# Kernel optimization log

Measured on AMD Instinct MI355X. Metric: run time of the kernel, lower is better.

## Reference

```python
import jax, jax.numpy as jnp
import numpy as np

IMG_SIZE = 416.0
CLASS_NUM = 80
NUM_ANCH = 3
MAX_GT = 64  # fixed padding for per-image valid GT boxes (original uses a variable-size python loop)


def _bce_logits(x, t):
    # BCEWithLogits, elementwise: softplus(x) - x*t  (numerically stable)
    return jax.nn.softplus(x) - x * t


def _make_noobj_mask(pred_boxes, targets):
    # pred_boxes: [B,G,G,3,4] in pixel units; targets: [B,G,G,3,85]
    B, G = pred_boxes.shape[0], pred_boxes.shape[1]
    N = G * G * NUM_ANCH
    conf = targets[..., 4].reshape(B, N)
    boxes = targets[..., 0:4].reshape(B, N, 4)
    # gather up to MAX_GT ground-truth boxes per image (conf>0 are the valid ones)
    top_conf, idx = jax.lax.top_k(conf, MAX_GT)            # [B,M]
    gt = jnp.take_along_axis(boxes, idx[..., None], axis=1)  # [B,M,4]
    valid = top_conf > 0.0                                   # [B,M]

    p = pred_boxes.reshape(B, N, 4)
    pxy = p[:, :, None, 0:2]   # [B,N,1,2]
    pwh = p[:, :, None, 2:4]
    gxy = gt[:, None, :, 0:2]  # [B,1,M,2]
    gwh = gt[:, None, :, 2:4]

    imin = jnp.maximum(pxy - pwh / 2, gxy - gwh / 2)
    imax = jnp.minimum(pxy + pwh / 2, gxy + gwh / 2)
    iwh = jnp.maximum(imax - imin, 0.0)
    inter = iwh[..., 0] * iwh[..., 1]                        # [B,N,M]
    area_p = pwh[..., 0] * pwh[..., 1]
    area_g = gwh[..., 0] * gwh[..., 1]
    iou = inter / (area_p + area_g - inter + 1e-9)
    iou = jnp.where(valid[:, None, :], iou, 0.0)
    best_iou = jnp.max(iou, axis=-1)                         # [B,N]
    noobj = (best_iou < 0.6).astype(pred_boxes.dtype)
    return noobj.reshape(B, G, G, NUM_ANCH)


def reference(preds, targets, anchors):
    B, G = preds.shape[0], preds.shape[1]
    ratio = IMG_SIZE / G
    p = preds.reshape(B, G, G, NUM_ANCH, 5 + CLASS_NUM)
    box_xy_raw, box_wh_raw, conf_logit, cls_logit = jnp.split(p, [2, 4, 5], axis=-1)

    # grid offsets: offset[i,j] = (j, i)
    gx, gy = jnp.meshgrid(jnp.arange(G, dtype=preds.dtype), jnp.arange(G, dtype=preds.dtype))
    offset = jnp.stack([gx, gy], axis=-1).reshape(G, G, 1, 2)

    sig_xy = jax.nn.sigmoid(box_xy_raw)
    box_xy = (sig_xy + offset) * ratio                 # pixel units
    box_wh = jnp.exp(box_wh_raw) * anchors             # (anchors/ratio)*ratio = anchors
    pred_boxes = jnp.concatenate([box_xy, box_wh], axis=-1)

    preds_xy = box_xy / ratio - offset                 # == sig_xy
    true_xy = targets[..., 0:2] / ratio - offset
    true_wh = targets[..., 2:4] / anchors
    preds_wh = box_wh / anchors
    true_wh = jnp.where(true_wh == 0.0, 1.0, true_wh)
    preds_wh = jnp.where(preds_wh == 0.0, 1.0, preds_wh)
    true_wh = jnp.log(jnp.clip(true_wh, 1e-9, 1e9))
    preds_wh = jnp.log(jnp.clip(preds_wh, 1e-9, 1e9))

    obj = (targets[..., 4] > 0.0).astype(preds.dtype)  # [B,G,G,3]
    obj_e = obj[..., None]
    scale = 2.0 - targets[..., 2:3] / IMG_SIZE * targets[..., 3:4] / IMG_SIZE  # [B,G,G,3,1]

    txty_loss = jnp.sum(obj_e * (preds_xy - true_xy) ** 2 * scale) / B
    twth_loss = jnp.sum(obj_e * (preds_wh - true_wh) ** 2 * scale) / B

    noobj = _make_noobj_mask(pred_boxes, targets)      # [B,G,G,3]
    noobj_conf_mask = (1.0 - obj) * noobj
    conf_t = targets[..., 4:5]
    noobj_conf_loss = jnp.sum(noobj_conf_mask[..., None] * _bce_logits(conf_logit, conf_t)) / B
    obj_conf_loss = jnp.sum(obj_e * _bce_logits(conf_logit, conf_t)) / B
    class_loss = jnp.sum(obj_e * _bce_logits(cls_logit, targets[..., 5:])) / B

    total_loss = txty_loss + twth_loss + noobj_conf_loss + obj_conf_loss + class_loss
    return (txty_loss, twth_loss, noobj_conf_loss, obj_conf_loss, class_loss, total_loss)


def setup_inputs() -> dict:
    key = jax.random.key(0)
    ks = jax.random.split(key, 5)
    B, G, A, C = 32, 52, NUM_ANCH, CLASS_NUM
    N = G * G * A
    M_OBJ = 40  # GT boxes per image (< MAX_GT)
    preds = jax.random.normal(ks[0], (B, G, G, A * (5 + C)), jnp.float32) * 0.5
    idx = jax.random.randint(ks[1], (B, M_OBJ), 0, N)
    xy = jax.random.uniform(ks[2], (B, M_OBJ, 2), jnp.float32, 0.0, IMG_SIZE)
    wh = jax.random.uniform(ks[3], (B, M_OBJ, 2), jnp.float32, 16.0, 128.0)
    cid = jax.random.randint(ks[4], (B, M_OBJ), 0, C)
    onehot = jax.nn.one_hot(cid, C, dtype=jnp.float32)
    vals = jnp.concatenate([xy, wh, jnp.ones((B, M_OBJ, 1), jnp.float32), onehot], axis=-1)
    t = jnp.zeros((B, N, 5 + C), jnp.float32)
    t = t.at[jnp.arange(B)[:, None], idx].set(vals)
    targets = t.reshape(B, G, G, A, 5 + C)
    anchors = jnp.array([[10.0, 13.0], [16.0, 30.0], [33.0, 23.0]], jnp.float32)
    return {"preds": preds, "targets": targets, "anchors": anchors}
```

## Files before the change

### kernel.cpp

```cpp
#include <hip/hip_runtime.h>
#include <math.h>

#define GSZ 52
#define NA 3
#define NCLS 80
#define CH 85
#define NCA (GSZ*GSZ*NA)
#define MAXGT 64
#define MCHUNK 32

__device__ __forceinline__ float softplus_fast(float x) {
    return fmaxf(x, 0.0f) + __logf(1.0f + __expf(-fabsf(x)));
}

__global__ void k_init(int* cnt, int B) {
    if (threadIdx.x < B) cnt[threadIdx.x] = 0;
}

__device__ __forceinline__ void emit_gt(const float* __restrict__ tg, size_t glob,
                                        int* cnt, float4* __restrict__ gtbox,
                                        int2* __restrict__ gtinfo) {
    const float* r = tg + glob * CH;
    int b    = (int)(glob / NCA);
    int nloc = (int)(glob - (size_t)b * NCA);
    int cid = 0;
#pragma unroll 16
    for (int c = 0; c < NCLS; c++) if (r[5 + c] > 0.5f) cid = c;
    int pos = atomicAdd(cnt + b, 1);
    if (pos < MAXGT) {
        gtbox[b * MAXGT + pos]  = make_float4(r[0], r[1], r[2], r[3]);
        gtinfo[b * MAXGT + pos] = make_int2(nloc, cid);
    }
}

__global__ void k_gt(const float* __restrict__ tg, int nrec, int* cnt,
                     float4* __restrict__ gtbox, int2* __restrict__ gtinfo) {
    int tid = threadIdx.x;
    size_t g0 = (size_t)blockIdx.x * 512 + tid;
    size_t g1 = g0 + 256;
    float c0 = (g0 < (size_t)nrec) ? tg[g0 * CH + 4] : 0.0f;
    float c1 = (g1 < (size_t)nrec) ? tg[g1 * CH + 4] : 0.0f;
    if (c0 > 0.0f) emit_gt(tg, g0, cnt, gtbox, gtinfo);
    if (c1 > 0.0f) emit_gt(tg, g1, cnt, gtbox, gtinfo);
}

__global__ void k_noobj(const float* __restrict__ pr,
                        const float* __restrict__ anchors,
                        const int* __restrict__ cnt,
                        const float4* __restrict__ gtbox,
                        const int2* __restrict__ gtinfo,
                        float* __restrict__ partial) {
    __shared__ float4 sbox[MAXGT];
    __shared__ int    sidx[MAXGT];
    __shared__ float  swsum[4];

    int b   = blockIdx.y;
    int tid = threadIdx.x;
    int n   = blockIdx.x * 256 + tid;

    int m = min(cnt[b], MAXGT);
    if (tid < m) {
        sbox[tid] = gtbox[b * MAXGT + tid];
        sidx[tid] = gtinfo[b * MAXGT + tid].x;
    }
    __syncthreads();

    float v = 0.0f;
    if (n < NCA) {
        const float* r = pr + ((size_t)b * NCA + n) * CH;
        float r0 = r[0], r1 = r[1], r2 = r[2], r3 = r[3], pc = r[4];

        int a    = n % NA;
        int cell = n / NA;
        int gi = cell / GSZ, gj = cell % GSZ;
        float aw = anchors[2 * a], ah = anchors[2 * a + 1];
        float sx = __builtin_amdgcn_rcpf(1.0f + __expf(-r0));
        float sy = __builtin_amdgcn_rcpf(1.0f + __expf(-r1));
        float bx = (sx + (float)gj) * 8.0f;
        float by = (sy + (float)gi) * 8.0f;
        float bw = __expf(r2) * aw;
        float bh = __expf(r3) * ah;

        float px0 = bx - bw * 0.5f, px1 = bx + bw * 0.5f;
        float py0 = by - bh * 0.5f, py1 = by + bh * 0.5f;
        float areap = bw * bh;

        float best = 0.0f;
        bool isobj = false;
        for (int k = 0; k < m; k++) {
            float4 g = sbox[k];
            isobj |= (sidx[k] == n);
            float ix = fminf(px1, g.x + g.z * 0.5f) - fmaxf(px0, g.x - g.z * 0.5f);
            float iy = fminf(py1, g.y + g.w * 0.5f) - fmaxf(py0, g.y - g.w * 0.5f);
            float inter = fmaxf(ix, 0.0f) * fmaxf(iy, 0.0f);
            float u = areap + g.z * g.w - inter + 1e-9f;
            best = fmaxf(best, inter * __builtin_amdgcn_rcpf(u));
        }
        if (!isobj && best < 0.6f) v = softplus_fast(pc);
    }

    int lane = tid & 63;
    int wv   = tid >> 6;
    for (int off = 32; off > 0; off >>= 1) v += __shfl_down(v, off);
    if (lane == 0) swsum[wv] = v;
    __syncthreads();
    if (tid == 0) {
        int bid = blockIdx.y * gridDim.x + blockIdx.x;
        partial[bid] = swsum[0] + swsum[1] + swsum[2] + swsum[3];
    }
}

__global__ void k_cls(const float* __restrict__ pr,
                      const float* __restrict__ anchors,
                      const int* __restrict__ cnt,
                      const float4* __restrict__ gtbox,
                      const int2* __restrict__ gtinfo,
                      float4* __restrict__ cls4) {
    int tid  = threadIdx.x;
    int wv   = tid >> 6;
    int lane = tid & 63;
    int slot = blockIdx.x * 4 + wv;
    int b = slot >> 6;
    int k = slot & (MAXGT - 1);

    float4 resv = make_float4(0.f, 0.f, 0.f, 0.f);
    int m = min(cnt[b], MAXGT);
    if (k < m) {
        float4 g  = gtbox[slot];
        int2 info = gtinfo[slot];
        int n = info.x, cid = info.y;
        size_t rec = (size_t)b * NCA + n;
        const float* rp = pr + rec * CH;
        const float* cl = rp + 5;

        float x0 = cl[lane];
        float cls = softplus_fast(x0) - (lane == cid ? x0 : 0.0f);
        if (lane < NCLS - 64) {
            float x1 = cl[64 + lane];
            cls += softplus_fast(x1) - ((64 + lane) == cid ? x1 : 0.0f);
        }
        for (int off = 32; off > 0; off >>= 1) cls += __shfl_down(cls, off);

        if (lane == 0) {
            float r0 = rp[0], r1 = rp[1], r2 = rp[2], r3 = rp[3], pc = rp[4];
            int a    = n % NA;
            int cell = n / NA;
            int gi = cell / GSZ, gj = cell % GSZ;
            float aw = anchors[2 * a], ah = anchors[2 * a + 1];

            float sx = __builtin_amdgcn_rcpf(1.0f + __expf(-r0));
            float sy = __builtin_amdgcn_rcpf(1.0f + __expf(-r1));
            float pbx = (sx + (float)gj) * 8.0f;
            float pby = (sy + (float)gi) * 8.0f;
            float pbz = __expf(r2) * aw;
            float pbw = __expf(r3) * ah;

            float scale = 2.0f - (g.z * (1.0f / 416.0f)) * (g.w * (1.0f / 416.0f));
            float dx = (pbx * 0.125f - (float)gj) - (g.x * 0.125f - (float)gj);
            float dy = (pby * 0.125f - (float)gi) - (g.y * 0.125f - (float)gi);
            float txty = (dx * dx + dy * dy) * scale;

            float rw = __builtin_amdgcn_rcpf(aw), rh = __builtin_amdgcn_rcpf(ah);
            float pwr = fminf(fmaxf(pbz * rw, 1e-9f), 1e9f);
            float phr = fminf(fmaxf(pbw * rh, 1e-9f), 1e9f);
            float twr = fminf(fmaxf(g.z  * rw, 1e-9f), 1e9f);
            float thr = fminf(fmaxf(g.w  * rh, 1e-9f), 1e9f);
            float dw = __logf(pwr) - __logf(twr);
            float dh = __logf(phr) - __logf(thr);
            float twth = (dw * dw + dh * dh) * scale;

            float obj = softplus_fast(pc) - pc;
            resv = make_float4(txty, twth, obj, cls);
        }
    }
    if (lane == 0) cls4[slot] = resv;
}

__global__ void k_final(const float* __restrict__ partial, int np,
                        const float4* __restrict__ cls4, int ns,
                        int B, float* __restrict__ out) {
    __shared__ double sred[4 * 5];
    int tid = threadIdx.x;
    double acc[5] = {0, 0, 0, 0, 0};
    for (int i = tid; i < np; i += 256) acc[2] += (double)partial[i];
    for (int i = tid; i < ns; i += 256) {
        float4 v = cls4[i];
        acc[0] += (double)v.x; acc[1] += (double)v.y;
        acc[3] += (double)v.z; acc[4] += (double)v.w;
    }
    int lane = tid & 63;
    int wv   = tid >> 6;
#pragma unroll
    for (int i = 0; i < 5; i++) {
        double v = acc[i];
        for (int off = 32; off > 0; off >>= 1) v += __shfl_down(v, off);
        if (lane == 0) sred[wv * 5 + i] = v;
    }
    __syncthreads();
    if (tid == 0) {
        double tot = 0.0;
#pragma unroll
        for (int i = 0; i < 5; i++) {
            double r = (sred[i] + sred[5 + i] + sred[10 + i] + sred[15 + i]) / (double)B;
            out[i] = (float)r;
            tot += r;
        }
        out[5] = (float)tot;
    }
}

extern "C" void kernel_launch(void* const* d_in, const int* in_sizes, int n_in,
                              void* d_out, int out_size, void* d_ws, size_t ws_size,
                              hipStream_t stream) {
    const float* preds   = (const float*)d_in[0];
    const float* targets = (const float*)d_in[1];
    const float* anchors = (const float*)d_in[2];
    float* out = (float*)d_out;

    int B = in_sizes[0] / (NCA * CH);
    int nrec = B * NCA;
    int gt_blocks = (nrec + 511) / 512;
    int np = MCHUNK * B;
    int ns = B * MAXGT;

    char* ws = (char*)d_ws;
    size_t off = 0;
    int*    cnt     = (int*)(ws + off);      off += 128;
    float4* gtbox   = (float4*)(ws + off);   off += (size_t)ns * sizeof(float4);
    int2*   gtinfo  = (int2*)(ws + off);     off += (size_t)ns * sizeof(int2);
    float*  partial = (float*)(ws + off);    off += (size_t)np * sizeof(float);
    off = (off + 15) & ~(size_t)15;
    float4* cls4    = (float4*)(ws + off);   off += (size_t)ns * sizeof(float4);

    k_init<<<1, 64, 0, stream>>>(cnt, B);
    k_gt<<<gt_blocks, 256, 0, stream>>>(targets, nrec, cnt, gtbox, gtinfo);
    dim3 grid(MCHUNK, B);
    k_noobj<<<grid, 256, 0, stream>>>(preds, anchors, cnt, gtbox, gtinfo, partial);
    k_cls<<<ns / 4, 256, 0, stream>>>(preds, anchors, cnt, gtbox, gtinfo, cls4);
    k_final<<<1, 256, 0, stream>>>(partial, np, cls4, ns, B, out);
}
```

Before: 197.1 us.

## Decode pred boxes during GT scan and merge noobj and class kernels

The GT-scan kernel now also reads the first five prediction channels of every record and writes the decoded box and confidence logit to a compact workspace. The noobj and class/box-loss kernels are merged into a single launch that reads these compact decoded values instead of the strided 85-float records. The aim is to cut one launch and turn strided prediction reads in the IoU pass into coalesced float4 reads. The cost is extra workspace traffic for the decoded arrays and a scan that now touches both input tensors.

Result: no change. 196.6 us (-0.2%).

```diff
diff --git a/kernel.cpp b/kernel.cpp
--- a/kernel.cpp
+++ b/kernel.cpp
@@ -8,6 +8,7 @@
 #define NCA (GSZ*GSZ*NA)
 #define MAXGT 64
 #define MCHUNK 32
+#define CLSBLK 16
 
 __device__ __forceinline__ float softplus_fast(float x) {
     return fmaxf(x, 0.0f) + __logf(1.0f + __expf(-fabsf(x)));
@@ -17,12 +18,12 @@
     if (threadIdx.x < B) cnt[threadIdx.x] = 0;
 }
 
-__device__ __forceinline__ void emit_gt(const float* __restrict__ tg, size_t glob,
+__device__ __forceinline__ void emit_gt(const float* __restrict__ tg, int glob,
                                         int* cnt, float4* __restrict__ gtbox,
                                         int2* __restrict__ gtinfo) {
-    const float* r = tg + glob * CH;
-    int b    = (int)(glob / NCA);
-    int nloc = (int)(glob - (size_t)b * NCA);
+    const float* r = tg + (size_t)glob * CH;
+    int b    = glob / NCA;
+    int nloc = glob - b * NCA;
     int cid = 0;
 #pragma unroll 16
     for (int c = 0; c < NCLS; c++) if (r[5 + c] > 0.5f) cid = c;
@@ -33,147 +34,144 @@
     }
 }
 
-__global__ void k_gt(const float* __restrict__ tg, int nrec, int* cnt,
-                     float4* __restrict__ gtbox, int2* __restrict__ gtinfo) {
-    int tid = threadIdx.x;
-    size_t g0 = (size_t)blockIdx.x * 512 + tid;
-    size_t g1 = g0 + 256;
-    float c0 = (g0 < (size_t)nrec) ? tg[g0 * CH + 4] : 0.0f;
-    float c1 = (g1 < (size_t)nrec) ? tg[g1 * CH + 4] : 0.0f;
-    if (c0 > 0.0f) emit_gt(tg, g0, cnt, gtbox, gtinfo);
-    if (c1 > 0.0f) emit_gt(tg, g1, cnt, gtbox, gtinfo);
-}
-
-__global__ void k_noobj(const float* __restrict__ pr,
-                        const float* __restrict__ anchors,
-                        const int* __restrict__ cnt,
-                        const float4* __restrict__ gtbox,
-                        const int2* __restrict__ gtinfo,
-                        float* __restrict__ partial) {
-    __shared__ float4 sbox[MAXGT];
-    __shared__ int    sidx[MAXGT];
-    __shared__ float  swsum[4];
-
+__global__ void k_scan(const float* __restrict__ tg, const float* __restrict__ pr,
+                       const float* __restrict__ anchors, int nrec, int* cnt,
+                       float4* __restrict__ gtbox, int2* __restrict__ gtinfo,
+                       float4* __restrict__ boxdec, float* __restrict__ confdec) {
+    int rec = blockIdx.x * 256 + threadIdx.x;
+    if (rec >= nrec) return;
+
+    float conf_t = tg[(size_t)rec * CH + 4];
+    const float* r = pr + (size_t)rec * CH;
+    float r0 = r[0], r1 = r[1], r2 = r[2], r3 = r[3], pc = r[4];
+
+    int b    = rec / NCA;
+    int n    = rec - b * NCA;
+    int a    = n % NA;
+    int cell = n / NA;
+    int gi = cell / GSZ, gj = cell % GSZ;
+    float aw = anchors[2 * a], ah = anchors[2 * a + 1];
+
+    float sx = __builtin_amdgcn_rcpf(1.0f + __expf(-r0));
+    float sy = __builtin_amdgcn_rcpf(1.0f + __expf(-r1));
+    float bx = (sx + (float)gj) * 8.0f;
+    float by = (sy + (float)gi) * 8.0f;
+    float bw = __expf(r2) * aw;
+    float bh = __expf(r3) * ah;
+
+    boxdec[rec]  = make_float4(bx, by, bw, bh);
+    confdec[rec] = pc;
+
+    if (conf_t > 0.0f) emit_gt(tg, rec, cnt, gtbox, gtinfo);
+}
+
+__global__ void k_nc(const float* __restrict__ pr,
+                     const float* __restrict__ anchors,
+                     const int* __restrict__ cnt,
+                     const float4* __restrict__ gtbox,
+                     const int2* __restrict__ gtinfo,
+                     const float4* __restrict__ boxdec,
+                     const float* __restrict__ confdec,
+                     float* __restrict__ partial,
+                     float4* __restrict__ cls4) {
     int b   = blockIdx.y;
     int tid = threadIdx.x;
-    int n   = blockIdx.x * 256 + tid;
-
-    int m = min(cnt[b], MAXGT);
-    if (tid < m) {
-        sbox[tid] = gtbox[b * MAXGT + tid];
-        sidx[tid] = gtinfo[b * MAXGT + tid].x;
-    }
-    __syncthreads();
-
-    float v = 0.0f;
-    if (n < NCA) {
-        const float* r = pr + ((size_t)b * NCA + n) * CH;
-        float r0 = r[0], r1 = r[1], r2 = r[2], r3 = r[3], pc = r[4];
-
-        int a    = n % NA;
-        int cell = n / NA;
-        int gi = cell / GSZ, gj = cell % GSZ;
-        float aw = anchors[2 * a], ah = anchors[2 * a + 1];
-        float sx = __builtin_amdgcn_rcpf(1.0f + __expf(-r0));
-        float sy = __builtin_amdgcn_rcpf(1.0f + __expf(-r1));
-        float bx = (sx + (float)gj) * 8.0f;
-        float by = (sy + (float)gi) * 8.0f;
-        float bw = __expf(r2) * aw;
-        float bh = __expf(r3) * ah;
-
-        float px0 = bx - bw * 0.5f, px1 = bx + bw * 0.5f;
-        float py0 = by - bh * 0.5f, py1 = by + bh * 0.5f;
-        float areap = bw * bh;
-
-        float best = 0.0f;
-        bool isobj = false;
-        for (int k = 0; k < m; k++) {
-            float4 g = sbox[k];
-            isobj |= (sidx[k] == n);
-            float ix = fminf(px1, g.x + g.z * 0.5f) - fmaxf(px0, g.x - g.z * 0.5f);
-            float iy = fminf(py1, g.y + g.w * 0.5f) - fmaxf(py0, g.y - g.w * 0.5f);
-            float inter = fmaxf(ix, 0.0f) * fmaxf(iy, 0.0f);
-            float u = areap + g.z * g.w - inter + 1e-9f;
-            best = fmaxf(best, inter * __builtin_amdgcn_rcpf(u));
-        }
-        if (!isobj && best < 0.6f) v = softplus_fast(pc);
-    }
-
-    int lane = tid & 63;
-    int wv   = tid >> 6;
-    for (int off = 32; off > 0; off >>= 1) v += __shfl_down(v, off);
-    if (lane == 0) swsum[wv] = v;
-    __syncthreads();
-    if (tid == 0) {
-        int bid = blockIdx.y * gridDim.x + blockIdx.x;
-        partial[bid] = swsum[0] + swsum[1] + swsum[2] + swsum[3];
-    }
-}
-
-__global__ void k_cls(const float* __restrict__ pr,
-                      const float* __restrict__ anchors,
-                      const int* __restrict__ cnt,
-                      const float4* __restrict__ gtbox,
-                      const int2* __restrict__ gtinfo,
-                      float4* __restrict__ cls4) {
-    int tid  = threadIdx.x;
-    int wv   = tid >> 6;
-    int lane = tid & 63;
-    int slot = blockIdx.x * 4 + wv;
-    int b = slot >> 6;
-    int k = slot & (MAXGT - 1);
-
-    float4 resv = make_float4(0.f, 0.f, 0.f, 0.f);
-    int m = min(cnt[b], MAXGT);
-    if (k < m) {
-        float4 g  = gtbox[slot];
-        int2 info = gtinfo[slot];
-        int n = info.x, cid = info.y;
-        size_t rec = (size_t)b * NCA + n;
-        const float* rp = pr + rec * CH;
-        const float* cl = rp + 5;
-
-        float x0 = cl[lane];
-        float cls = softplus_fast(x0) - (lane == cid ? x0 : 0.0f);
-        if (lane < NCLS - 64) {
-            float x1 = cl[64 + lane];
-            cls += softplus_fast(x1) - ((64 + lane) == cid ? x1 : 0.0f);
-        }
-        for (int off = 32; off > 0; off >>= 1) cls += __shfl_down(cls, off);
-
-        if (lane == 0) {
-            float r0 = rp[0], r1 = rp[1], r2 = rp[2], r3 = rp[3], pc = rp[4];
-            int a    = n % NA;
-            int cell = n / NA;
-            int gi = cell / GSZ, gj = cell % GSZ;
-            float aw = anchors[2 * a], ah = anchors[2 * a + 1];
-
-            float sx = __builtin_amdgcn_rcpf(1.0f + __expf(-r0));
-            float sy = __builtin_amdgcn_rcpf(1.0f + __expf(-r1));
-            float pbx = (sx + (float)gj) * 8.0f;
-            float pby = (sy + (float)gi) * 8.0f;
-            float pbz = __expf(r2) * aw;
-            float pbw = __expf(r3) * ah;
-
-            float scale = 2.0f - (g.z * (1.0f / 416.0f)) * (g.w * (1.0f / 416.0f));
-            float dx = (pbx * 0.125f - (float)gj) - (g.x * 0.125f - (float)gj);
-            float dy = (pby * 0.125f - (float)gi) - (g.y * 0.125f - (float)gi);
-            float txty = (dx * dx + dy * dy) * scale;
-
-            float rw = __builtin_amdgcn_rcpf(aw), rh = __builtin_amdgcn_rcpf(ah);
-            float pwr = fminf(fmaxf(pbz * rw, 1e-9f), 1e9f);
-            float phr = fminf(fmaxf(pbw * rh, 1e-9f), 1e9f);
-            float twr = fminf(fmaxf(g.z  * rw, 1e-9f), 1e9f);
-            float thr = fminf(fmaxf(g.w  * rh, 1e-9f), 1e9f);
-            float dw = __logf(pwr) - __logf(twr);
-            float dh = __logf(phr) - __logf(thr);
-            float twth = (dw * dw + dh * dh) * scale;
-
-            float obj = softplus_fast(pc) - pc;
-            resv = make_float4(txty, twth, obj, cls);
-        }
-    }
-    if (lane == 0) cls4[slot] = resv;
+
+    if (blockIdx.x < MCHUNK) {
+        __shared__ float4 sbox[MAXGT];
+        __shared__ int    sidx[MAXGT];
+        __shared__ float  swsum[4];
+
+        int n = blockIdx.x * 256 + tid;
+        int m = min(cnt[b], MAXGT);
+        if (tid < m) {
+            sbox[tid] = gtbox[b * MAXGT + tid];
+            sidx[tid] = gtinfo[b * MAXGT + tid].x;
+        }
+        __syncthreads();
+
+        float v = 0.0f;
+        if (n < NCA) {
+            size_t rec = (size_t)b * NCA + n;
+            float4 pb = boxdec[rec];
+            float  pc = confdec[rec];
+            float px0 = pb.x - pb.z * 0.5f, px1 = pb.x + pb.z * 0.5f;
+            float py0 = pb.y - pb.w * 0.5f, py1 = pb.y + pb.w * 0.5f;
+            float areap = pb.z * pb.w;
+
+            float best = 0.0f;
+            bool isobj = false;
+            for (int k = 0; k < m; k++) {
+                float4 g = sbox[k];
+                isobj |= (sidx[k] == n);
+                float ix = fminf(px1, g.x + g.z * 0.5f) - fmaxf(px0, g.x - g.z * 0.5f);
+                float iy = fminf(py1, g.y + g.w * 0.5f) - fmaxf(py0, g.y - g.w * 0.5f);
+                float inter = fmaxf(ix, 0.0f) * fmaxf(iy, 0.0f);
+                float u = areap + g.z * g.w - inter + 1e-9f;
+                best = fmaxf(best, inter * __builtin_amdgcn_rcpf(u));
+            }
+            if (!isobj && best < 0.6f) v = softplus_fast(pc);
+        }
+
+        int lane = tid & 63;
+        int wv   = tid >> 6;
+        for (int off = 32; off > 0; off >>= 1) v += __shfl_down(v, off);
+        if (lane == 0) swsum[wv] = v;
+        __syncthreads();
+        if (tid == 0) {
+            partial[b * MCHUNK + blockIdx.x] = swsum[0] + swsum[1] + swsum[2] + swsum[3];
+        }
+    } else {
+        int wv   = tid >> 6;
+        int lane = tid & 63;
+        int slot = b * MAXGT + (blockIdx.x - MCHUNK) * 4 + wv;
+        int k    = slot & (MAXGT - 1);
+
+        float4 resv = make_float4(0.f, 0.f, 0.f, 0.f);
+        int m = min(cnt[b], MAXGT);
+        if (k < m) {
+            float4 g  = gtbox[slot];
+            int2 info = gtinfo[slot];
+            int n = info.x, cid = info.y;
+            size_t rec = (size_t)b * NCA + n;
+            const float* cl = pr + rec * CH + 5;
+
+            float x0 = cl[lane];
+            float cls = softplus_fast(x0) - (lane == cid ? x0 : 0.0f);
+            if (lane < NCLS - 64) {
+                float x1 = cl[64 + lane];
+                cls += softplus_fast(x1) - ((64 + lane) == cid ? x1 : 0.0f);
+            }
+            for (int off = 32; off > 0; off >>= 1) cls += __shfl_down(cls, off);
+
+            if (lane == 0) {
+                float4 pb = boxdec[rec];
+                float  pc = confdec[rec];
+                int a    = n % NA;
+                int cell = n / NA;
+                int gi = cell / GSZ, gj = cell % GSZ;
+                float aw = anchors[2 * a], ah = anchors[2 * a + 1];
+
+                float scale = 2.0f - (g.z * (1.0f / 416.0f)) * (g.w * (1.0f / 416.0f));
+                float dx = (pb.x * 0.125f - (float)gj) - (g.x * 0.125f - (float)gj);
+                float dy = (pb.y * 0.125f - (float)gi) - (g.y * 0.125f - (float)gi);
+                float txty = (dx * dx + dy * dy) * scale;
+
+                float rw = __builtin_amdgcn_rcpf(aw), rh = __builtin_amdgcn_rcpf(ah);
+                float pwr = fminf(fmaxf(pb.z * rw, 1e-9f), 1e9f);
+                float phr = fminf(fmaxf(pb.w * rh, 1e-9f), 1e9f);
+                float twr = fminf(fmaxf(g.z  * rw, 1e-9f), 1e9f);
+                float thr = fminf(fmaxf(g.w  * rh, 1e-9f), 1e9f);
+                float dw = __logf(pwr) - __logf(twr);
+                float dh = __logf(phr) - __logf(thr);
+                float twth = (dw * dw + dh * dh) * scale;
+
+                float obj = softplus_fast(pc) - pc;
+                resv = make_float4(txty, twth, obj, cls);
+            }
+        }
+        if (lane == 0) cls4[slot] = resv;
+    }
 }
 
 __global__ void k_final(const float* __restrict__ partial, int np,
@@ -219,7 +217,7 @@
 
     int B = in_sizes[0] / (NCA * CH);
     int nrec = B * NCA;
-    int gt_blocks = (nrec + 511) / 512;
+    int scan_blocks = (nrec + 255) / 256;
     int np = MCHUNK * B;
     int ns = B * MAXGT;
 
@@ -230,12 +228,16 @@
     int2*   gtinfo  = (int2*)(ws + off);     off += (size_t)ns * sizeof(int2);
     float*  partial = (float*)(ws + off);    off += (size_t)np * sizeof(float);
     off = (off + 15) & ~(size_t)15;
+    float4* boxdec  = (float4*)(ws + off);   off += (size_t)nrec * sizeof(float4);
+    float*  confdec = (float*)(ws + off);    off += (size_t)nrec * sizeof(float);
+    off = (off + 15) & ~(size_t)15;
     float4* cls4    = (float4*)(ws + off);   off += (size_t)ns * sizeof(float4);
 
     k_init<<<1, 64, 0, stream>>>(cnt, B);
-    k_gt<<<gt_blocks, 256, 0, stream>>>(targets, nrec, cnt, gtbox, gtinfo);
-    dim3 grid(MCHUNK, B);
-    k_noobj<<<grid, 256, 0, stream>>>(preds, anchors, cnt, gtbox, gtinfo, partial);
-    k_cls<<<ns / 4, 256, 0, stream>>>(preds, anchors, cnt, gtbox, gtinfo, cls4);
+    k_scan<<<scan_blocks, 256, 0, stream>>>(targets, preds, anchors, nrec, cnt,
+                                            gtbox, gtinfo, boxdec, confdec);
+    dim3 grid(MCHUNK + CLSBLK, B);
+    k_nc<<<grid, 256, 0, stream>>>(preds, anchors, cnt, gtbox, gtinfo,
+                                   boxdec, confdec, partial, cls4);
     k_final<<<1, 256, 0, stream>>>(partial, np, cls4, ns, B, out);
 }
```
